# Performance work log

Measured on AMD Instinct MI355X. Metric: run time of the kernel, lower is better.

Reference implementation:

```python
import jax, jax.numpy as jnp
import numpy as np


def setup_inputs() -> dict:
    key = jax.random.key(0)
    kq, kk, kv = jax.random.split(key, 3)
    B, S, H, D = 2, 2048, 32, 128
    q = jax.random.normal(kq, (B, S, H, D), dtype=jnp.float32)
    k = jax.random.normal(kk, (B, S, H, D), dtype=jnp.float32)
    v = jax.random.normal(kv, (B, S, H, D), dtype=jnp.float32)
    return {"q": q, "k": k, "v": v}


def _causal_attention(q, k, v):
    # q,k,v: [B, S, H, D] (flash-attn layout). Zigzag ring attention computes
    # exactly standard causal attention; zigzag only balances work across ranks.
    B, S, H, D = q.shape
    scale = 1.0 / jnp.sqrt(jnp.asarray(D, q.dtype))
    scores = jnp.einsum('bqhd,bkhd->bhqk', q, k) * scale  # [B,H,S,S]
    causal = jnp.tril(jnp.ones((S, S), dtype=bool))
    scores = jnp.where(causal, scores, jnp.finfo(scores.dtype).min)
    probs = jax.nn.softmax(scores, axis=-1)
    return jnp.einsum('bhqk,bkhd->bqhd', probs, v)  # [B,S,H,D]


def reference(q, k, v):
    out = _causal_attention(q, k, v)
    return jnp.sum(out)
```

## Files before the change

kernel.cpp:

```cpp
#include <hip/hip_runtime.h>
#include <hip/hip_bf16.h>
#include <stdint.h>

#define B_ 2
#define S_ 2048
#define H_ 32
#define D_ 128
#define R_ (B_*H_*S_)
#define PG 2048
#define CPB 27

typedef __bf16 bf16x8 __attribute__((ext_vector_type(8)));
typedef float  f32x16 __attribute__((ext_vector_type(16)));

#if __has_builtin(__builtin_amdgcn_exp2f)
#define EXP2F(x) __builtin_amdgcn_exp2f(x)
#else
#define EXP2F(x) exp2f(x)
#endif

#define AS1 __attribute__((address_space(1)))
#define AS3 __attribute__((address_space(3)))

__device__ __forceinline__ unsigned short f2bf(float f) {
  unsigned u = __float_as_uint(f);
  u += 0x7FFFu + ((u >> 16) & 1u);
  return (unsigned short)(u >> 16);
}

__global__ __launch_bounds__(256) void prep(
    const float* __restrict__ qf, const float* __restrict__ kf,
    const float* __restrict__ v,
    unsigned short* __restrict__ qc, unsigned short* __restrict__ kc,
    float* __restrict__ vsum, float* __restrict__ nd, float* __restrict__ out0) {
  const int bid = blockIdx.x;
  const int t = threadIdx.x;
  if (bid == 0 && t == 0) out0[0] = 0.f;
  const float sc = 0.0883883476483184f * 1.4426950408889634f;
  const size_t i0 = (size_t)bid * 256 + t;

  float4 rq[8], rk[8];
  #pragma unroll
  for (int g = 0; g < 8; ++g)
    rq[g] = reinterpret_cast<const float4*>(qf)[(size_t)g * (PG * 256) + i0];
  #pragma unroll
  for (int g = 0; g < 8; ++g)
    rk[g] = reinterpret_cast<const float4*>(kf)[(size_t)g * (PG * 256) + i0];
  __builtin_amdgcn_sched_barrier(0);

  #pragma unroll
  for (int g = 0; g < 8; ++g) {
    ushort4 o;
    o.x = f2bf(rq[g].x * sc); o.y = f2bf(rq[g].y * sc);
    o.z = f2bf(rq[g].z * sc); o.w = f2bf(rq[g].w * sc);
    reinterpret_cast<ushort4*>(qc)[(size_t)g * (PG * 256) + i0] = o;
  }
  #pragma unroll
  for (int g = 0; g < 8; ++g) {
    ushort4 o;
    o.x = f2bf(rk[g].x); o.y = f2bf(rk[g].y);
    o.z = f2bf(rk[g].z); o.w = f2bf(rk[g].w);
    reinterpret_cast<ushort4*>(kc)[(size_t)g * (PG * 256) + i0] = o;
  }

  {
    float4 rv[8];
    #pragma unroll
    for (int g = 0; g < 2; ++g) {
      const int u = bid + g * PG;
      const int b = u / S_, s = u % S_;
      const float4* panel =
          reinterpret_cast<const float4*>(v + (((size_t)b * S_ + s) * H_) * D_);
      #pragma unroll
      for (int j = 0; j < 4; ++j) rv[g * 4 + j] = panel[j * 256 + t];
    }
    __builtin_amdgcn_sched_barrier(0);
    #pragma unroll
    for (int g = 0; g < 2; ++g) {
      const int u = bid + g * PG;
      const int b = u / S_, s = u % S_;
      #pragma unroll
      for (int j = 0; j < 4; ++j) {
        const float4 a = rv[g * 4 + j];
        float sum = a.x + a.y + a.z + a.w;
        sum += __shfl_xor(sum, 1);
        sum += __shfl_xor(sum, 2);
        sum += __shfl_xor(sum, 4);
        sum += __shfl_xor(sum, 8);
        sum += __shfl_xor(sum, 16);
        const int h = j * 8 + (t >> 5);
        if ((t & 31) == 0) vsum[((size_t)b * H_ + h) * S_ + s] = sum;
      }
    }
  }
  if (bid < 256) {
    float4* p = reinterpret_cast<float4*>(nd);
    p[(size_t)bid * 256 + t] = float4{0.f, 0.f, 0.f, 0.f};
  }
}

__global__ __launch_bounds__(256, 3) void attn_sum(
    const unsigned short* __restrict__ qc, const unsigned short* __restrict__ kc,
    const float* __restrict__ vsum, float* __restrict__ numb,
    float* __restrict__ denb) {
  __shared__ uint4 kbuf[4][512];
  __shared__ float vsbuf[4][64];

  const int id = blockIdx.x;
  const int y  = id >> 3;
  const int bh = (id & 7) + 8 * (y / CPB);
  const int c  = y % CPB;

  int g, h, nch;
  if (c < 1)       { g = 0; h = c;      nch = 1; }
  else if (c < 3)  { g = 1; h = c - 1;  nch = 2; }
  else if (c < 5)  { g = 2; h = c - 3;  nch = 2; }
  else if (c < 8)  { g = 3; h = c - 5;  nch = 3; }
  else if (c < 12) { g = 4; h = c - 8;  nch = 4; }
  else if (c < 16) { g = 5; h = c - 12; nch = 4; }
  else if (c < 21) { g = 6; h = c - 16; nch = 5; }
  else             { g = 7; h = c - 21; nch = 6; }
  const int nkt  = 4 * g + 4;
  const int bas_ = nkt / nch, rem = nkt % nch;
  const int kt0  = h * bas_ + (h < rem ? h : rem);
  const int kt1  = kt0 + bas_ + (h < rem ? 1 : 0);
  const int st0  = 2 * kt0, st1 = 2 * kt1;

  const int t  = threadIdx.x;
  const int w  = t >> 6;
  const int l  = t & 63;
  const int ln = l & 31, l5 = l >> 5;

  const int b0 = bh >> 5, h0 = bh & 31;
  const int qminA = (2 * g) * 128 + w * 32;
  const int qminB = (2 * g + 1) * 128 + w * 32;
  const unsigned short* kc0 = kc + ((size_t)b0 * S_ * H_ + h0) * D_;
  const float* vsrc0 = vsum + (size_t)bh * S_;

  bf16x8 qfA[8], qfB[8];
  {
    const unsigned short* qpA =
        qc + (((size_t)b0 * S_ + qminA + ln) * H_ + h0) * D_ + l5 * 8;
    const unsigned short* qpB =
        qc + (((size_t)b0 * S_ + qminB + ln) * H_ + h0) * D_ + l5 * 8;
    #pragma unroll
    for (int kb8 = 0; kb8 < 8; ++kb8) {
      qfA[kb8] = *reinterpret_cast<const bf16x8*>(qpA + kb8 * 16);
      qfB[kb8] = *reinterpret_cast<const bf16x8*>(qpB + kb8 * 16);
    }
  }

  auto stage = [&](int st, int slot) {
    #pragma unroll
    for (int j = 0; j < 2; ++j) {
      const int idx = (w * 2 + j) * 64 + l;
      const int r   = idx >> 4;
      const int p   = idx & 15;
      const int cc  = p ^ (r & 15);
      const unsigned short* src = kc0 + (size_t)(st * 32 + r) * (H_ * D_) + cc * 8;
      __builtin_amdgcn_global_load_lds(
          (const AS1 void*)src, (AS3 void*)(&kbuf[slot][idx & ~63]), 16, 0, 0);
    }
    __builtin_amdgcn_global_load_lds(
        (const AS1 void*)(vsrc0 + st * 32 + l), (AS3 void*)(&vsbuf[slot][0]), 4, 0, 0);
  };

  float npA = 0.f, dpA = 0.f, npB = 0.f, dpB = 0.f;

  stage(st0, st0 & 3);
  stage(st0 + 1, (st0 + 1) & 3);

  const int xr = ln & 15;
  for (int st = st0; st < st1; ++st) {
    if (st + 1 < st1) asm volatile("s_waitcnt vmcnt(3)" ::: "memory");
    else              asm volatile("s_waitcnt vmcnt(0)" ::: "memory");
    __builtin_amdgcn_s_barrier();
    if (st + 2 < st1) stage(st + 2, (st + 2) & 3);

    const int kbase = st * 32;
    if (kbase <= qminB + 31) {
      const int slot = st & 3;
      const uint4* rowb = &kbuf[slot][ln * 16];
      bf16x8 kf[8];
      #pragma unroll
      for (int kb8 = 0; kb8 < 8; ++kb8)
        kf[kb8] = *reinterpret_cast<const bf16x8*>(&rowb[(kb8 * 2 + l5) ^ xr]);
      const float4 vs0 = *reinterpret_cast<const float4*>(&vsbuf[slot][ 0 + 4 * l5]);
      const float4 vs1 = *reinterpret_cast<const float4*>(&vsbuf[slot][ 8 + 4 * l5]);
      const float4 vs2 = *reinterpret_cast<const float4*>(&vsbuf[slot][16 + 4 * l5]);
      const float4 vs3 = *reinterpret_cast<const float4*>(&vsbuf[slot][24 + 4 * l5]);
      const float vsa[16] = {vs0.x,vs0.y,vs0.z,vs0.w, vs1.x,vs1.y,vs1.z,vs1.w,
                             vs2.x,vs2.y,vs2.z,vs2.w, vs3.x,vs3.y,vs3.z,vs3.w};

      {
        f32x16 sacc = {0.f,0.f,0.f,0.f,0.f,0.f,0.f,0.f,
                       0.f,0.f,0.f,0.f,0.f,0.f,0.f,0.f};
        __builtin_amdgcn_s_setprio(1);
        #pragma unroll
        for (int kb8 = 0; kb8 < 8; ++kb8)
          sacc = __builtin_amdgcn_mfma_f32_32x32x16_bf16(kf[kb8], qfB[kb8], sacc, 0, 0, 0);
        __builtin_amdgcn_s_setprio(0);
        if (kbase + 31 <= qminB) {
          #pragma unroll
          for (int r = 0; r < 16; ++r) {
            const float e = EXP2F(sacc[r]);
            dpB += e;
            npB = fmaf(e, vsa[r], npB);
          }
        } else {
          const int qg = qminB + ln;
          #pragma unroll
          for (int r = 0; r < 16; ++r) {
            const int kr = kbase + (r & 3) + 8 * (r >> 2) + 4 * l5;
            const float e = (kr <= qg) ? EXP2F(sacc[r]) : 0.f;
            dpB += e;
            npB = fmaf(e, vsa[r], npB);
          }
        }
      }
      if (kbase <= qminA + 31) {
        f32x16 sacc = {0.f,0.f,0.f,0.f,0.f,0.f,0.f,0.f,
                       0.f,0.f,0.f,0.f,0.f,0.f,0.f,0.f};
        __builtin_amdgcn_s_setprio(1);
        #pragma unroll
        for (int kb8 = 0; kb8 < 8; ++kb8)
          sacc = __builtin_amdgcn_mfma_f32_32x32x16_bf16(kf[kb8], qfA[kb8], sacc, 0, 0, 0);
        __builtin_amdgcn_s_setprio(0);
        if (kbase + 31 <= qminA) {
          #pragma unroll
          for (int r = 0; r < 16; ++r) {
            const float e = EXP2F(sacc[r]);
            dpA += e;
            npA = fmaf(e, vsa[r], npA);
          }
        } else {
          const int qg = qminA + ln;
          #pragma unroll
          for (int r = 0; r < 16; ++r) {
            const int kr = kbase + (r & 3) + 8 * (r >> 2) + 4 * l5;
            const float e = (kr <= qg) ? EXP2F(sacc[r]) : 0.f;
            dpA += e;
            npA = fmaf(e, vsa[r], npA);
          }
        }
      }
    }
  }

  npA += __shfl_xor(npA, 32); dpA += __shfl_xor(dpA, 32);
  npB += __shfl_xor(npB, 32); dpB += __shfl_xor(dpB, 32);
  if (l5 == 0) {
    float* nrow = numb + (size_t)bh * S_;
    float* drow = denb + (size_t)bh * S_;
    atomicAdd(&nrow[qminA + ln], npA);
    atomicAdd(&drow[qminA + ln], dpA);
    atomicAdd(&nrow[qminB + ln], npB);
    atomicAdd(&drow[qminB + ln], dpB);
  }
}

__global__ __launch_bounds__(256) void finalize(
    const float* __restrict__ numb, const float* __restrict__ denb,
    float* __restrict__ out) {
  const int i = blockIdx.x * 256 + threadIdx.x;
  float c = numb[i] / denb[i];
  #pragma unroll
  for (int m = 1; m < 64; m <<= 1) c += __shfl_xor(c, m);
  __shared__ float ps[4];
  if ((threadIdx.x & 63) == 0) ps[threadIdx.x >> 6] = c;
  __syncthreads();
  if (threadIdx.x == 0) atomicAdd(out, ps[0] + ps[1] + ps[2] + ps[3]);
}

extern "C" void kernel_launch(void* const* d_in, const int* in_sizes, int n_in,
                              void* d_out, int out_size, void* d_ws, size_t ws_size,
                              hipStream_t stream) {
  const float* q = (const float*)d_in[0];
  const float* k = (const float*)d_in[1];
  const float* v = (const float*)d_in[2];
  float* out = (float*)d_out;

  unsigned short* qc = (unsigned short*)d_ws;
  unsigned short* kc = qc + (size_t)R_ * D_;
  float* vsum = (float*)(kc + (size_t)R_ * D_);
  float* numb = vsum + R_;
  float* denb = numb + R_;

  hipLaunchKernelGGL(prep, dim3(PG), dim3(256), 0, stream,
                     q, k, v, qc, kc, vsum, numb, out);
  hipLaunchKernelGGL(attn_sum, dim3(64 * CPB), dim3(256), 0, stream,
                     qc, kc, vsum, numb, denb);
  hipLaunchKernelGGL(finalize, dim3(R_ / 256), dim3(256), 0, stream,
                     numb, denb, out);
}
```

Measured before the change: 105.6 us.

## Fuse q/k bf16 conversion into attention kernel, drop prep conversion pass

Removes the separate pass in the prep kernel that converted q and k from fp32 to bf16 into workspace buffers. The attention kernel now reads fp32 q directly and converts it with v_cvt_pk_bf16_f32, and streams fp32 K tiles into LDS, converting them to bf16 right before the MFMAs. This saves a full read/write round trip of the converted q and k buffers. In exchange, K global traffic per block doubles, K staging LDS doubles (slots reduced from 4 to 3), and conversion VALU work is added to the inner loop.

After: 125.8 us. 1.19x slower.

```diff
diff --git a/kernel.cpp b/kernel.cpp
--- a/kernel.cpp
+++ b/kernel.cpp
@@ -22,75 +22,36 @@
 #define AS1 __attribute__((address_space(1)))
 #define AS3 __attribute__((address_space(3)))
 
-__device__ __forceinline__ unsigned short f2bf(float f) {
-  unsigned u = __float_as_uint(f);
-  u += 0x7FFFu + ((u >> 16) & 1u);
-  return (unsigned short)(u >> 16);
+__device__ __forceinline__ unsigned int cvtpk(float a, float b) {
+  unsigned int r;
+  asm("v_cvt_pk_bf16_f32 %0, %1, %2" : "=v"(r) : "v"(a), "v"(b));
+  return r;
 }
 
 __global__ __launch_bounds__(256) void prep(
-    const float* __restrict__ qf, const float* __restrict__ kf,
-    const float* __restrict__ v,
-    unsigned short* __restrict__ qc, unsigned short* __restrict__ kc,
-    float* __restrict__ vsum, float* __restrict__ nd, float* __restrict__ out0) {
+    const float* __restrict__ v, float* __restrict__ vsum,
+    float* __restrict__ nd, float* __restrict__ out0) {
   const int bid = blockIdx.x;
   const int t = threadIdx.x;
   if (bid == 0 && t == 0) out0[0] = 0.f;
-  const float sc = 0.0883883476483184f * 1.4426950408889634f;
-  const size_t i0 = (size_t)bid * 256 + t;
-
-  float4 rq[8], rk[8];
+
   #pragma unroll
-  for (int g = 0; g < 8; ++g)
-    rq[g] = reinterpret_cast<const float4*>(qf)[(size_t)g * (PG * 256) + i0];
-  #pragma unroll
-  for (int g = 0; g < 8; ++g)
-    rk[g] = reinterpret_cast<const float4*>(kf)[(size_t)g * (PG * 256) + i0];
-  __builtin_amdgcn_sched_barrier(0);
-
-  #pragma unroll
-  for (int g = 0; g < 8; ++g) {
-    ushort4 o;
-    o.x = f2bf(rq[g].x * sc); o.y = f2bf(rq[g].y * sc);
-    o.z = f2bf(rq[g].z * sc); o.w = f2bf(rq[g].w * sc);
-    reinterpret_cast<ushort4*>(qc)[(size_t)g * (PG * 256) + i0] = o;
-  }
-  #pragma unroll
-  for (int g = 0; g < 8; ++g) {
-    ushort4 o;
-    o.x = f2bf(rk[g].x); o.y = f2bf(rk[g].y);
-    o.z = f2bf(rk[g].z); o.w = f2bf(rk[g].w);
-    reinterpret_cast<ushort4*>(kc)[(size_t)g * (PG * 256) + i0] = o;
-  }
-
-  {
-    float4 rv[8];
+  for (int g = 0; g < (B_ * S_) / PG; ++g) {
+    const int u = bid + g * PG;
+    const int b = u / S_, s = u % S_;
+    const float4* panel =
+        reinterpret_cast<const float4*>(v + (((size_t)b * S_ + s) * H_) * D_);
     #pragma unroll
-    for (int g = 0; g < 2; ++g) {
-      const int u = bid + g * PG;
-      const int b = u / S_, s = u % S_;
-      const float4* panel =
-          reinterpret_cast<const float4*>(v + (((size_t)b * S_ + s) * H_) * D_);
-      #pragma unroll
-      for (int j = 0; j < 4; ++j) rv[g * 4 + j] = panel[j * 256 + t];
-    }
-    __builtin_amdgcn_sched_barrier(0);
-    #pragma unroll
-    for (int g = 0; g < 2; ++g) {
-      const int u = bid + g * PG;
-      const int b = u / S_, s = u % S_;
-      #pragma unroll
-      for (int j = 0; j < 4; ++j) {
-        const float4 a = rv[g * 4 + j];
-        float sum = a.x + a.y + a.z + a.w;
-        sum += __shfl_xor(sum, 1);
-        sum += __shfl_xor(sum, 2);
-        sum += __shfl_xor(sum, 4);
-        sum += __shfl_xor(sum, 8);
-        sum += __shfl_xor(sum, 16);
-        const int h = j * 8 + (t >> 5);
-        if ((t & 31) == 0) vsum[((size_t)b * H_ + h) * S_ + s] = sum;
-      }
+    for (int j = 0; j < 4; ++j) {
+      const float4 a = panel[j * 256 + t];
+      float sum = a.x + a.y + a.z + a.w;
+      sum += __shfl_xor(sum, 1);
+      sum += __shfl_xor(sum, 2);
+      sum += __shfl_xor(sum, 4);
+      sum += __shfl_xor(sum, 8);
+      sum += __shfl_xor(sum, 16);
+      const int h = j * 8 + (t >> 5);
+      if ((t & 31) == 0) vsum[((size_t)b * H_ + h) * S_ + s] = sum;
     }
   }
   if (bid < 256) {
@@ -100,11 +61,11 @@
 }
 
 __global__ __launch_bounds__(256, 3) void attn_sum(
-    const unsigned short* __restrict__ qc, const unsigned short* __restrict__ kc,
+    const float* __restrict__ qf, const float* __restrict__ kf,
     const float* __restrict__ vsum, float* __restrict__ numb,
     float* __restrict__ denb) {
-  __shared__ uint4 kbuf[4][512];
-  __shared__ float vsbuf[4][64];
+  __shared__ float kbufF[3][32 * 128];
+  __shared__ float vsbuf[3][64];
 
   const int id = blockIdx.x;
   const int y  = id >> 3;
@@ -134,32 +95,42 @@
   const int b0 = bh >> 5, h0 = bh & 31;
   const int qminA = (2 * g) * 128 + w * 32;
   const int qminB = (2 * g + 1) * 128 + w * 32;
-  const unsigned short* kc0 = kc + ((size_t)b0 * S_ * H_ + h0) * D_;
+  const float* kf0 = kf + ((size_t)b0 * S_ * H_ + h0) * D_;
   const float* vsrc0 = vsum + (size_t)bh * S_;
 
+  const float sc = 0.0883883476483184f * 1.4426950408889634f;
   bf16x8 qfA[8], qfB[8];
   {
-    const unsigned short* qpA =
-        qc + (((size_t)b0 * S_ + qminA + ln) * H_ + h0) * D_ + l5 * 8;
-    const unsigned short* qpB =
-        qc + (((size_t)b0 * S_ + qminB + ln) * H_ + h0) * D_ + l5 * 8;
+    const float* qpA = qf + (((size_t)b0 * S_ + qminA + ln) * H_ + h0) * D_ + l5 * 8;
+    const float* qpB = qf + (((size_t)b0 * S_ + qminB + ln) * H_ + h0) * D_ + l5 * 8;
     #pragma unroll
     for (int kb8 = 0; kb8 < 8; ++kb8) {
-      qfA[kb8] = *reinterpret_cast<const bf16x8*>(qpA + kb8 * 16);
-      qfB[kb8] = *reinterpret_cast<const bf16x8*>(qpB + kb8 * 16);
+      float4 a = *reinterpret_cast<const float4*>(qpA + kb8 * 16);
+      float4 b = *reinterpret_cast<const float4*>(qpA + kb8 * 16 + 4);
+      union { unsigned int u[4]; bf16x8 v; } oA;
+      oA.u[0] = cvtpk(a.x * sc, a.y * sc); oA.u[1] = cvtpk(a.z * sc, a.w * sc);
+      oA.u[2] = cvtpk(b.x * sc, b.y * sc); oA.u[3] = cvtpk(b.z * sc, b.w * sc);
+      qfA[kb8] = oA.v;
+      a = *reinterpret_cast<const float4*>(qpB + kb8 * 16);
+      b = *reinterpret_cast<const float4*>(qpB + kb8 * 16 + 4);
+      union { unsigned int u[4]; bf16x8 v; } oB;
+      oB.u[0] = cvtpk(a.x * sc, a.y * sc); oB.u[1] = cvtpk(a.z * sc, a.w * sc);
+      oB.u[2] = cvtpk(b.x * sc, b.y * sc); oB.u[3] = cvtpk(b.z * sc, b.w * sc);
+      qfB[kb8] = oB.v;
     }
   }
 
   auto stage = [&](int st, int slot) {
     #pragma unroll
-    for (int j = 0; j < 2; ++j) {
-      const int idx = (w * 2 + j) * 64 + l;
-      const int r   = idx >> 4;
-      const int p   = idx & 15;
-      const int cc  = p ^ (r & 15);
-      const unsigned short* src = kc0 + (size_t)(st * 32 + r) * (H_ * D_) + cc * 8;
+    for (int j = 0; j < 4; ++j) {
+      const int idx = (w * 4 + j) * 64 + l;
+      const int r   = idx >> 5;
+      const int p   = idx & 31;
+      const int cc  = p ^ (r & 31);
+      const float* src = kf0 + (size_t)(st * 32 + r) * (H_ * D_) + cc * 4;
       __builtin_amdgcn_global_load_lds(
-          (const AS1 void*)src, (AS3 void*)(&kbuf[slot][idx & ~63]), 16, 0, 0);
+          (const AS1 void*)src,
+          (AS3 void*)(&kbufF[slot][(idx & ~63) * 4]), 16, 0, 0);
     }
     __builtin_amdgcn_global_load_lds(
         (const AS1 void*)(vsrc0 + st * 32 + l), (AS3 void*)(&vsbuf[slot][0]), 4, 0, 0);
@@ -167,24 +138,32 @@
 
   float npA = 0.f, dpA = 0.f, npB = 0.f, dpB = 0.f;
 
-  stage(st0, st0 & 3);
-  stage(st0 + 1, (st0 + 1) & 3);
-
-  const int xr = ln & 15;
+  stage(st0, st0 % 3);
+  stage(st0 + 1, (st0 + 1) % 3);
+
+  const int xr = ln & 31;
   for (int st = st0; st < st1; ++st) {
-    if (st + 1 < st1) asm volatile("s_waitcnt vmcnt(3)" ::: "memory");
+    if (st + 1 < st1) asm volatile("s_waitcnt vmcnt(5)" ::: "memory");
     else              asm volatile("s_waitcnt vmcnt(0)" ::: "memory");
     __builtin_amdgcn_s_barrier();
-    if (st + 2 < st1) stage(st + 2, (st + 2) & 3);
+    if (st + 2 < st1) stage(st + 2, (st + 2) % 3);
 
     const int kbase = st * 32;
     if (kbase <= qminB + 31) {
-      const int slot = st & 3;
-      const uint4* rowb = &kbuf[slot][ln * 16];
-      bf16x8 kf[8];
+      const int slot = st % 3;
+      const float4* rowb =
+          reinterpret_cast<const float4*>(&kbufF[slot][ln * 128]);
+      bf16x8 kfr[8];
       #pragma unroll
-      for (int kb8 = 0; kb8 < 8; ++kb8)
-        kf[kb8] = *reinterpret_cast<const bf16x8*>(&rowb[(kb8 * 2 + l5) ^ xr]);
+      for (int kb8 = 0; kb8 < 8; ++kb8) {
+        const int c0 = kb8 * 4 + l5 * 2;
+        const float4 u0 = rowb[c0 ^ xr];
+        const float4 u1 = rowb[(c0 + 1) ^ xr];
+        union { unsigned int u[4]; bf16x8 v; } o;
+        o.u[0] = cvtpk(u0.x, u0.y); o.u[1] = cvtpk(u0.z, u0.w);
+        o.u[2] = cvtpk(u1.x, u1.y); o.u[3] = cvtpk(u1.z, u1.w);
+        kfr[kb8] = o.v;
+      }
       const float4 vs0 = *reinterpret_cast<const float4*>(&vsbuf[slot][ 0 + 4 * l5]);
       const float4 vs1 = *reinterpret_cast<const float4*>(&vsbuf[slot][ 8 + 4 * l5]);
       const float4 vs2 = *reinterpret_cast<const float4*>(&vsbuf[slot][16 + 4 * l5]);
@@ -198,7 +177,7 @@
         __builtin_amdgcn_s_setprio(1);
         #pragma unroll
         for (int kb8 = 0; kb8 < 8; ++kb8)
-          sacc = __builtin_amdgcn_mfma_f32_32x32x16_bf16(kf[kb8], qfB[kb8], sacc, 0, 0, 0);
+          sacc = __builtin_amdgcn_mfma_f32_32x32x16_bf16(kfr[kb8], qfB[kb8], sacc, 0, 0, 0);
         __builtin_amdgcn_s_setprio(0);
         if (kbase + 31 <= qminB) {
           #pragma unroll
@@ -224,7 +203,7 @@
         __builtin_amdgcn_s_setprio(1);
         #pragma unroll
         for (int kb8 = 0; kb8 < 8; ++kb8)
-          sacc = __builtin_amdgcn_mfma_f32_32x32x16_bf16(kf[kb8], qfA[kb8], sacc, 0, 0, 0);
+          sacc = __builtin_amdgcn_mfma_f32_32x32x16_bf16(kfr[kb8], qfA[kb8], sacc, 0, 0, 0);
         __builtin_amdgcn_s_setprio(0);
         if (kbase + 31 <= qminA) {
           #pragma unroll
@@ -280,16 +259,14 @@
   const float* v = (const float*)d_in[2];
   float* out = (float*)d_out;
 
-  unsigned short* qc = (unsigned short*)d_ws;
-  unsigned short* kc = qc + (size_t)R_ * D_;
-  float* vsum = (float*)(kc + (size_t)R_ * D_);
+  float* vsum = (float*)d_ws;
   float* numb = vsum + R_;
   float* denb = numb + R_;
 
   hipLaunchKernelGGL(prep, dim3(PG), dim3(256), 0, stream,
-                     q, k, v, qc, kc, vsum, numb, out);
+                     v, vsum, numb, out);
   hipLaunchKernelGGL(attn_sum, dim3(64 * CPB), dim3(256), 0, stream,
-                     qc, kc, vsum, numb, denb);
+                     q, k, vsum, numb, denb);
   hipLaunchKernelGGL(finalize, dim3(R_ / 256), dim3(256), 0, stream,
                      numb, denb, out);
 }
```
